# Optimization experiments

Measured on AMD Instinct MI355X. Metric: run time of the kernel, lower is better.

## Reference

```python
import jax, jax.numpy as jnp
import numpy as np

N, E, G, D, L, EA = 100000, 1600000, 128, 128, 3, 7
BN_EPS = 1e-5


def _bn(x, g, b, m, v):
    # eval-mode BatchNorm1d with running stats
    return (x - m) * (g / jnp.sqrt(v + BN_EPS)) + b


def setup_inputs() -> dict:
    key = jax.random.key(0)
    ks = iter(jax.random.split(key, 64))
    nrm = lambda shape, s: jax.random.normal(next(ks), shape, jnp.float32) * s
    unif = lambda shape: jax.random.uniform(next(ks), shape, jnp.float32) * 0.5 + 0.5
    inp = {
        # forward tensor args
        'x': jnp.zeros((N,), jnp.int32),  # indices into Embedding(1, D) -> all zero
        'edge_index': jax.random.randint(next(ks), (2, E), 0, N, jnp.int32),
        'edge_attr': nrm((E, EA), 1.0),
        'batch': jnp.sort(jax.random.randint(next(ks), (N,), 0, G, jnp.int32)),
        # embeddings
        'node_emb': nrm((1, D), 1.0),
        'vn_emb': nrm((1, D), 0.1),
        # per-layer GINConv params (stacked on leading layer dim)
        'edge_W': nrm((L, EA, D), EA ** -0.5), 'edge_b': jnp.zeros((L, D), jnp.float32),
        'eps': jnp.zeros((L,), jnp.float32),
        'mlp_W1': nrm((L, D, 2 * D), D ** -0.5), 'mlp_b1': jnp.zeros((L, 2 * D), jnp.float32),
        'mbn_g': jnp.ones((L, 2 * D), jnp.float32), 'mbn_b': jnp.zeros((L, 2 * D), jnp.float32),
        'mbn_m': nrm((L, 2 * D), 0.1), 'mbn_v': unif((L, 2 * D)),
        'mlp_W2': nrm((L, 2 * D, D), (2 * D) ** -0.5), 'mlp_b2': jnp.zeros((L, D), jnp.float32),
        # outer per-layer BatchNorm
        'bn_g': jnp.ones((L, D), jnp.float32), 'bn_b': jnp.zeros((L, D), jnp.float32),
        'bn_m': nrm((L, D), 0.1), 'bn_v': unif((L, D)),
        # virtual-node MLPs (L-1 of them)
        'vn_W1': nrm((L - 1, D, 2 * D), D ** -0.5), 'vn_b1': jnp.zeros((L - 1, 2 * D), jnp.float32),
        'vbn1_g': jnp.ones((L - 1, 2 * D), jnp.float32), 'vbn1_b': jnp.zeros((L - 1, 2 * D), jnp.float32),
        'vbn1_m': nrm((L - 1, 2 * D), 0.1), 'vbn1_v': unif((L - 1, 2 * D)),
        'vn_W2': nrm((L - 1, 2 * D, D), (2 * D) ** -0.5), 'vn_b2': jnp.zeros((L - 1, D), jnp.float32),
        'vbn2_g': jnp.ones((L - 1, D), jnp.float32), 'vbn2_b': jnp.zeros((L - 1, D), jnp.float32),
        'vbn2_m': nrm((L - 1, D), 0.1), 'vbn2_v': unif((L - 1, D)),
    }
    return inp


def reference(x, edge_index, edge_attr, batch, node_emb, vn_emb,
              edge_W, edge_b, eps, mlp_W1, mlp_b1, mbn_g, mbn_b, mbn_m, mbn_v,
              mlp_W2, mlp_b2, bn_g, bn_b, bn_m, bn_v,
              vn_W1, vn_b1, vbn1_g, vbn1_b, vbn1_m, vbn1_v,
              vn_W2, vn_b2, vbn2_g, vbn2_b, vbn2_m, vbn2_v):
    src, dst = edge_index[0], edge_index[1]
    h = node_emb[x]                                # [N, D] node encoder gather
    vn = jnp.broadcast_to(vn_emb[0], (G, D))       # virtual node per graph
    for l in range(L):
        h_in = h + vn[batch]                       # broadcast virtual node to nodes
        # GINConv
        e = edge_attr @ edge_W[l] + edge_b[l]      # [E, D]
        msg = jax.nn.relu(h_in[src] + e)           # gather + edge fuse
        agg = jax.ops.segment_sum(msg, dst, num_segments=N)
        z = (1.0 + eps[l]) * h_in + agg
        z = jax.nn.relu(_bn(z @ mlp_W1[l] + mlp_b1[l], mbn_g[l], mbn_b[l], mbn_m[l], mbn_v[l]))
        h2 = z @ mlp_W2[l] + mlp_b2[l]
        # outer BatchNorm (+ relu except last layer; dropout is identity in eval)
        h2 = _bn(h2, bn_g[l], bn_b[l], bn_m[l], bn_v[l])
        h = h2 if l == L - 1 else jax.nn.relu(h2)
        if l < L - 1:
            vt = jax.ops.segment_sum(h_in, batch, num_segments=G) + vn  # global_add_pool
            t = jax.nn.relu(_bn(vt @ vn_W1[l] + vn_b1[l], vbn1_g[l], vbn1_b[l], vbn1_m[l], vbn1_v[l]))
            vn = jax.nn.relu(_bn(t @ vn_W2[l] + vn_b2[l], vbn2_g[l], vbn2_b[l], vbn2_m[l], vbn2_v[l]))
    return h  # JK == 'last'
```

## Files before the change

### kernel.cpp

```cpp
#include <hip/hip_runtime.h>
#include <hip/hip_bf16.h>

#define NN 100000
#define NP 100032
#define EE 1600000
#define GG 128
#define DD 128
#define LL 3
#define EAA 7
#define BN_EPS 1e-5f

typedef __attribute__((ext_vector_type(8))) short bf16x8;
typedef __attribute__((ext_vector_type(4))) float f32x4;
typedef __attribute__((ext_vector_type(4))) unsigned short u16x4;

__device__ __forceinline__ unsigned short f2bf(float x) {
    unsigned int u = __float_as_uint(x);
    u = (u + 0x7FFF + ((u >> 16) & 1)) >> 16;
    return (unsigned short)u;
}
__device__ __forceinline__ float bf2f(unsigned short h) {
    return __uint_as_float(((unsigned int)h) << 16);
}
__device__ __forceinline__ float bflo(unsigned int u) {
    return __uint_as_float(u << 16);
}
__device__ __forceinline__ float bfhi(unsigned int u) {
    return __uint_as_float(u & 0xFFFF0000u);
}

__global__ __launch_bounds__(256) void init_kernel(
    const int* __restrict__ x, const float* __restrict__ node_emb,
    const float* __restrict__ vn_emb, float* __restrict__ h,
    float* __restrict__ vn)
{
    long i = (long)blockIdx.x * 256 + threadIdx.x;
    if (i < (long)NN * DD) {
        int node = (int)(i >> 7), d = (int)(i & 127);
        h[i] = node_emb[(long)x[node] * DD + d];
    }
    if (i < GG * DD) vn[i] = vn_emb[i & 127];
}

#define R1 8
__global__ __launch_bounds__(256) void hin_kernel(
    float* __restrict__ hbuf,
    unsigned short* __restrict__ h16,
    const float* __restrict__ vn,
    const int* __restrict__ batch,
    const float* __restrict__ eps,
    float* __restrict__ agg,
    float* __restrict__ vt,
    int layer, int accum_vt, int write_agg)
{
    const int d  = threadIdx.x & 127;
    const int rg = threadIdx.x >> 7;
    const float epl = 1.0f + eps[layer];
    const long row0 = (long)blockIdx.x * (R1 * 2);

    float vacc = 0.0f;
    int   vb   = -1;
    #pragma unroll
    for (int r = 0; r < R1; ++r) {
        long row = row0 + rg + 2 * r;
        if (row >= NN) break;
        int b = batch[row];
        long idx = row * DD + d;
        float hv = hbuf[idx] + vn[(long)b * DD + d];
        hbuf[idx] = hv;
        h16[idx]  = f2bf(hv);
        if (write_agg) agg[idx] = epl * hv;
        if (accum_vt) {
            if (b != vb) {
                if (vb >= 0) atomicAdd(&vt[(long)vb * DD + d], vacc);
                vb = b; vacc = 0.0f;
            }
            vacc += hv;
        }
    }
    if (accum_vt && vb >= 0) atomicAdd(&vt[(long)vb * DD + d], vacc);
}

__global__ __launch_bounds__(256) void vt_kernel(
    const float* __restrict__ hbuf, const int* __restrict__ batch,
    float* __restrict__ vt)
{
    const int d  = threadIdx.x & 127;
    const int rg = threadIdx.x >> 7;
    const long row0 = (long)blockIdx.x * 16;
    float vacc = 0.0f;
    int   vb   = -1;
    #pragma unroll
    for (int r = 0; r < 8; ++r) {
        long row = row0 + rg + 2 * r;
        if (row >= NN) break;
        int b = batch[row];
        float hv = hbuf[row * DD + d];
        if (b != vb) {
            if (vb >= 0) atomicAdd(&vt[(long)vb * DD + d], vacc);
            vb = b; vacc = 0.0f;
        }
        vacc += hv;
    }
    if (vb >= 0) atomicAdd(&vt[(long)vb * DD + d], vacc);
}

__global__ __launch_bounds__(256) void cnt_kernel(
    const int* __restrict__ batch, int* __restrict__ cnt)
{
    const int tid = blockIdx.x * 256 + threadIdx.x;
    const int CH  = (NN + 16383) / 16384;
    long s = (long)tid * CH;
    long e = s + CH; if (e > NN) e = NN;
    int vb = -1, c = 0;
    for (long i = s; i < e; ++i) {
        int b = batch[i];
        if (b != vb) { if (vb >= 0) atomicAdd(&cnt[vb], c); vb = b; c = 0; }
        ++c;
    }
    if (vb >= 0) atomicAdd(&cnt[vb], c);
}

__global__ __launch_bounds__(256) void count_kernel(
    const int* __restrict__ ei, int* __restrict__ deg)
{
    long e = (long)blockIdx.x * 256 + threadIdx.x;
    if (e < EE) atomicAdd(&deg[ei[EE + e]], 1);
}

__global__ __launch_bounds__(1024) void scan_a(
    const int* __restrict__ deg, int* __restrict__ rp, int* __restrict__ partials)
{
    __shared__ int s[1024];
    int t = threadIdx.x;
    long i = (long)blockIdx.x * 1024 + t;
    int v = (i < NN) ? deg[i] : 0;
    s[t] = v;
    __syncthreads();
    for (int off = 1; off < 1024; off <<= 1) {
        int u = (t >= off) ? s[t - off] : 0;
        __syncthreads();
        s[t] += u;
        __syncthreads();
    }
    if (i < NN) rp[i] = s[t] - v;
    if (t == 1023) partials[blockIdx.x] = s[1023];
}

__global__ void scan_b(int* __restrict__ partials, int nb)
{
    if (threadIdx.x == 0) {
        int run = 0;
        for (int i = 0; i < nb; ++i) { int v = partials[i]; partials[i] = run; run += v; }
    }
}

__global__ __launch_bounds__(1024) void scan_c(
    int* __restrict__ rp, int* __restrict__ fill, const int* __restrict__ partials)
{
    long i = (long)blockIdx.x * 1024 + threadIdx.x;
    if (i < NN) {
        int v = rp[i] + partials[blockIdx.x];
        rp[i] = v;
        fill[i] = v;
    }
    if (i == 0) rp[NN] = EE;
}

__global__ __launch_bounds__(256) void scatter_kernel(
    const int* __restrict__ ei, const float* __restrict__ eattr,
    int* __restrict__ fill, unsigned short* __restrict__ attr16,
    int* __restrict__ src_arr, int* __restrict__ eid_perm)
{
    long e = (long)blockIdx.x * 256 + threadIdx.x;
    if (e >= EE) return;
    int dst = ei[EE + e];
    int pos = atomicAdd(&fill[dst], 1);
    if (attr16) {
        u16x4 w0, w1;
        w0.x = f2bf(eattr[e * EAA + 0]);
        w0.y = f2bf(eattr[e * EAA + 1]);
        w0.z = f2bf(eattr[e * EAA + 2]);
        w0.w = f2bf(eattr[e * EAA + 3]);
        w1.x = f2bf(eattr[e * EAA + 4]);
        w1.y = f2bf(eattr[e * EAA + 5]);
        w1.z = f2bf(eattr[e * EAA + 6]);
        w1.w = 0;
        *(u16x4*)(attr16 + (long)pos * 8)     = w0;
        *(u16x4*)(attr16 + (long)pos * 8 + 4) = w1;
        src_arr[pos] = ei[e];
    } else {
        eid_perm[pos] = (int)e;
    }
}

__global__ __launch_bounds__(256) void gin0_kernel(
    const float* __restrict__ node_emb,
    const float* __restrict__ vn_emb,
    const int* __restrict__ rp,
    const unsigned short* __restrict__ attr16,
    const float* __restrict__ eW, const float* __restrict__ eb,
    const float* __restrict__ eps,
    float* __restrict__ agg)
{
    const int lane = threadIdx.x & 63;
    const int wid  = threadIdx.x >> 6;
    const long n   = (long)blockIdx.x * 4 + wid;
    const int d0   = lane * 2;

    float2 w2[EAA];
    #pragma unroll
    for (int a = 0; a < EAA; ++a)
        w2[a] = *(const float2*)&eW[a * DD + d0];
    const float2 bias = *(const float2*)&eb[d0];
    const float  epl  = 1.0f + eps[0];

    const float cx = node_emb[d0]     + vn_emb[d0];
    const float cy = node_emb[d0 + 1] + vn_emb[d0 + 1];
    float accx = epl * cx, accy = epl * cy;

    int p  = rp[n];
    const int p1 = rp[n + 1];

    #define EDGE0(AU)                                                         \
    {                                                                         \
        float a0 = bflo(AU.x), a1 = bfhi(AU.x);                               \
        float a2 = bflo(AU.y), a3 = bfhi(AU.y);                               \
        float a4 = bflo(AU.z), a5 = bfhi(AU.z);                               \
        float a6 = bflo(AU.w);                                                \
        float ex = bias.x, ey = bias.y;                                       \
        ex = fmaf(a0, w2[0].x, ex); ey = fmaf(a0, w2[0].y, ey);               \
        ex = fmaf(a1, w2[1].x, ex); ey = fmaf(a1, w2[1].y, ey);               \
        ex = fmaf(a2, w2[2].x, ex); ey = fmaf(a2, w2[2].y, ey);               \
        ex = fmaf(a3, w2[3].x, ex); ey = fmaf(a3, w2[3].y, ey);               \
        ex = fmaf(a4, w2[4].x, ex); ey = fmaf(a4, w2[4].y, ey);               \
        ex = fmaf(a5, w2[5].x, ex); ey = fmaf(a5, w2[5].y, ey);               \
        ex = fmaf(a6, w2[6].x, ex); ey = fmaf(a6, w2[6].y, ey);               \
        float mx = cx + ex, my = cy + ey;                                     \
        accx += fmaxf(mx, 0.0f); accy += fmaxf(my, 0.0f);                     \
    }

    for (; p + 4 <= p1; p += 4) {
        const uint4* a4p = (const uint4*)(attr16 + (long)p * 8);
        uint4 A0 = a4p[0];
        uint4 A1 = a4p[1];
        uint4 A2 = a4p[2];
        uint4 A3 = a4p[3];
        EDGE0(A0)
        EDGE0(A1)
        EDGE0(A2)
        EDGE0(A3)
    }
    for (; p < p1; ++p) {
        uint4 A = *(const uint4*)(attr16 + (long)p * 8);
        EDGE0(A)
    }
    #undef EDGE0

    *(float2*)&agg[n * DD + d0] = make_float2(accx, accy);
}

__global__ __launch_bounds__(256) void gin_agg_kernel(
    const float* __restrict__ h_in,
    const unsigned short* __restrict__ h16,
    const int* __restrict__ rp,
    const unsigned short* __restrict__ attr16,
    const int* __restrict__ src_arr,
    const float* __restrict__ eW, const float* __restrict__ eb,
    const float* __restrict__ eps,
    float* __restrict__ agg, int layer)
{
    const int lane = threadIdx.x & 63;
    const int wid  = threadIdx.x >> 6;
    const long n   = (long)blockIdx.x * 4 + wid;
    const int d0   = lane * 2;

    const float* eWl = eW + (long)layer * EAA * DD;
    float2 w2[EAA];
    #pragma unroll
    for (int a = 0; a < EAA; ++a)
        w2[a] = *(const float2*)&eWl[a * DD + d0];
    const float2 bias = *(const float2*)&eb[layer * DD + d0];
    const float  epl  = 1.0f + eps[layer];

    float2 hn = *(const float2*)&h_in[n * DD + d0];
    float accx = epl * hn.x, accy = epl * hn.y;

    int p  = rp[n];
    const int p1 = rp[n + 1];

    #define EDGE(AU, GU)                                                      \
    {                                                                         \
        float a0 = bflo(AU.x), a1 = bfhi(AU.x);                               \
        float a2 = bflo(AU.y), a3 = bfhi(AU.y);                               \
        float a4 = bflo(AU.z), a5 = bfhi(AU.z);                               \
        float a6 = bflo(AU.w);                                                \
        float ex = bias.x, ey = bias.y;                                       \
        ex = fmaf(a0, w2[0].x, ex); ey = fmaf(a0, w2[0].y, ey);               \
        ex = fmaf(a1, w2[1].x, ex); ey = fmaf(a1, w2[1].y, ey);               \
        ex = fmaf(a2, w2[2].x, ex); ey = fmaf(a2, w2[2].y, ey);               \
        ex = fmaf(a3, w2[3].x, ex); ey = fmaf(a3, w2[3].y, ey);               \
        ex = fmaf(a4, w2[4].x, ex); ey = fmaf(a4, w2[4].y, ey);               \
        ex = fmaf(a5, w2[5].x, ex); ey = fmaf(a5, w2[5].y, ey);               \
        ex = fmaf(a6, w2[6].x, ex); ey = fmaf(a6, w2[6].y, ey);               \
        float mx = bflo(GU) + ex, my = bfhi(GU) + ey;                         \
        accx += fmaxf(mx, 0.0f); accy += fmaxf(my, 0.0f);                     \
    }

    for (; p + 4 <= p1; p += 4) {
        int s0 = src_arr[p];
        int s1 = src_arr[p + 1];
        int s2 = src_arr[p + 2];
        int s3 = src_arr[p + 3];
        const uint4* a4p = (const uint4*)(attr16 + (long)p * 8);
        uint4 A0 = a4p[0];
        uint4 A1 = a4p[1];
        uint4 A2 = a4p[2];
        uint4 A3 = a4p[3];
        unsigned int g0 = *(const unsigned int*)(h16 + (long)s0 * DD + d0);
        unsigned int g1 = *(const unsigned int*)(h16 + (long)s1 * DD + d0);
        unsigned int g2 = *(const unsigned int*)(h16 + (long)s2 * DD + d0);
        unsigned int g3 = *(const unsigned int*)(h16 + (long)s3 * DD + d0);
        EDGE(A0, g0)
        EDGE(A1, g1)
        EDGE(A2, g2)
        EDGE(A3, g3)
    }
    for (; p < p1; ++p) {
        int s = src_arr[p];
        uint4 A = *(const uint4*)(attr16 + (long)p * 8);
        unsigned int g = *(const unsigned int*)(h16 + (long)s * DD + d0);
        EDGE(A, g)
    }
    #undef EDGE

    *(float2*)&agg[n * DD + d0] = make_float2(accx, accy);
}

__global__ __launch_bounds__(256) void gin_agg_eid_kernel(
    const float* __restrict__ h_in,
    const int* __restrict__ rp,
    const int* __restrict__ eid_perm,
    const int* __restrict__ ei,
    const float* __restrict__ eattr,
    const float* __restrict__ eW, const float* __restrict__ eb,
    const float* __restrict__ eps,
    float* __restrict__ agg, int layer)
{
    const int d    = threadIdx.x & 127;
    const int half = threadIdx.x >> 7;
    const long n   = (long)blockIdx.x * 2 + half;

    float w[EAA];
    #pragma unroll
    for (int a = 0; a < EAA; ++a) w[a] = eW[layer * EAA * DD + a * DD + d];
    const float bias = eb[layer * DD + d];
    const float epl  = 1.0f + eps[layer];

    float acc = epl * h_in[n * DD + d];
    const int p0 = rp[n], p1 = rp[n + 1];
    for (int p = p0; p < p1; ++p) {
        int e = eid_perm[p];
        int src = ei[e];
        float ea = bias;
        #pragma unroll
        for (int a = 0; a < EAA; ++a)
            ea = fmaf(eattr[(long)e * EAA + a], w[a], ea);
        float m = h_in[(long)src * DD + d] + ea;
        acc += m > 0.0f ? m : 0.0f;
    }
    agg[n * DD + d] = acc;
}

#define EPB 64
__global__ __launch_bounds__(256) void edge_kernel(
    const float* __restrict__ h_in,
    const int* __restrict__ ei,
    const float* __restrict__ eattr,
    const float* __restrict__ eW,
    const float* __restrict__ eb,
    float* __restrict__ agg,
    int layer)
{
    const int d    = threadIdx.x & 127;
    const int esub = threadIdx.x >> 7;
    float w[EAA];
    #pragma unroll
    for (int a = 0; a < EAA; ++a) w[a] = eW[layer * EAA * DD + a * DD + d];
    const float bias = eb[layer * DD + d];

    const long base = (long)blockIdx.x * EPB;
    for (int k = esub; k < EPB; k += 2) {
        long e = base + k;
        if (e >= EE) break;
        int s = ei[e];
        int t = ei[EE + e];
        float acc = bias;
        #pragma unroll
        for (int a = 0; a < EAA; ++a)
            acc = fmaf(eattr[e * EAA + a], w[a], acc);
        float m = h_in[(long)s * DD + d] + acc;
        m = m > 0.0f ? m : 0.0f;
        atomicAdd(&agg[(long)t * DD + d], m);
    }
}

__global__ __launch_bounds__(256) void wprep_kernel(
    const float* __restrict__ W1, const float* __restrict__ W2,
    unsigned short* __restrict__ w1h, unsigned short* __restrict__ w1l,
    unsigned short* __restrict__ w2h, unsigned short* __restrict__ w2l)
{
    int tid = blockIdx.x * 256 + threadIdx.x;
    if (tid >= LL * 2 * 32768) return;
    int l = tid / 65536;
    int rem = tid - l * 65536;
    int mat = rem >> 15;
    int fi = rem & 32767;
    int b = fi & 7, lane = (fi >> 3) & 63;
    int kgrp = ((lane >> 4) << 3) + b;
    if (mat == 0) {
        int mt = (fi >> 9) & 15, kk = fi >> 13;
        int m = (mt << 4) + (lane & 15);
        int k = (kk << 5) + kgrp;
        float v = W1[(long)l * DD * 2 * DD + (long)k * 2 * DD + m];
        unsigned short hi = f2bf(v);
        w1h[(long)l * 32768 + fi] = hi;
        w1l[(long)l * 32768 + fi] = f2bf(v - bf2f(hi));
    } else {
        int mt = (fi >> 9) & 7, kk = fi >> 12;
        int m = (mt << 4) + (lane & 15);
        int k = (kk << 5) + kgrp;
        float v = W2[(long)l * 2 * DD * DD + (long)k * DD + m];
        unsigned short hi = f2bf(v);
        w2h[(long)l * 32768 + fi] = hi;
        w2l[(long)l * 32768 + fi] = f2bf(v - bf2f(hi));
    }
}

__global__ __launch_bounds__(256) void bnprep_kernel(
    const float* __restrict__ b1, const float* __restrict__ g1,
    const float* __restrict__ be1, const float* __restrict__ m1,
    const float* __restrict__ v1,
    const float* __restrict__ b2, const float* __restrict__ g2,
    const float* __restrict__ be2, const float* __restrict__ m2,
    const float* __restrict__ v2,
    float* __restrict__ sc1, float* __restrict__ sh1,
    float* __restrict__ sc2, float* __restrict__ sh2)
{
    int tid = blockIdx.x * 256 + threadIdx.x;
    if (tid < LL * 2 * DD) {
        float sc = g1[tid] / sqrtf(v1[tid] + BN_EPS);
        sc1[tid] = sc;
        sh1[tid] = (b1[tid] - m1[tid]) * sc + be1[tid];
    }
    int t2 = tid - LL * 2 * DD;
    if (t2 >= 0 && t2 < LL * DD) {
        float sc = g2[t2] / sqrtf(v2[t2] + BN_EPS);
        sc2[t2] = sc;
        sh2[t2] = (b2[t2] - m2[t2]) * sc + be2[t2];
    }
}

__global__ __launch_bounds__(256, 2) void mlp_mfma_kernel(
    const float* __restrict__ z_in,
    const unsigned short* __restrict__ w1h, const unsigned short* __restrict__ w1l,
    const unsigned short* __restrict__ w2h, const unsigned short* __restrict__ w2l,
    const float* __restrict__ sc1, const float* __restrict__ sh1,
    const float* __restrict__ sc2, const float* __restrict__ sh2,
    float* __restrict__ h_out, int layer, int do_relu,
    const int* __restrict__ batch, const float* __restrict__ vnbuf,
    unsigned short* __restrict__ h16, int fuse)
{
    __shared__ char lds[65536];
    const int tid  = threadIdx.x;
    const int lane = tid & 63;
    const int wv   = tid >> 6;
    const long row0 = (long)blockIdx.x * 64;
    const int kb = (lane >> 4) << 3;

    {
        const float4* zi = (const float4*)(z_in + row0 * DD);
        #pragma unroll
        for (int i = 0; i < 8; ++i) {
            int idx = tid + i * 256;
            float4 v = zi[idx];
            int r = idx >> 5;
            int c = (idx & 31) << 2;
            u16x4 hv, lv;
            hv.x = f2bf(v.x); lv.x = f2bf(v.x - bf2f(hv.x));
            hv.y = f2bf(v.y); lv.y = f2bf(v.y - bf2f(hv.y));
            hv.z = f2bf(v.z); lv.z = f2bf(v.z - bf2f(hv.z));
            hv.w = f2bf(v.w); lv.w = f2bf(v.w - bf2f(hv.w));
            int off = ((r << 8) + (c << 1)) ^ ((r & 7) << 4);
            *(u16x4*)(lds + off)         = hv;
            *(u16x4*)(lds + 16384 + off) = lv;
        }
    }
    __syncthreads();

    bf16x8 B1h[4][4], B1l[4][4];
    #pragma unroll
    for (int nt = 0; nt < 4; ++nt) {
        int r = (nt << 4) + (lane & 15);
        #pragma unroll
        for (int kk = 0; kk < 4; ++kk) {
            int off = ((r << 8) + (((kk << 5) + kb) << 1)) ^ ((r & 7) << 4);
            B1h[nt][kk] = *(const bf16x8*)(lds + off);
            B1l[nt][kk] = *(const bf16x8*)(lds + 16384 + off);
        }
    }
    __syncthreads();

    const unsigned short* w1hl = w1h + (long)layer * 32768;
    const unsigned short* w1ll = w1l + (long)layer * 32768;
    #pragma unroll
    for (int mtl = 0; mtl < 4; ++mtl) {
        const int mt = (wv << 2) + mtl;
        bf16x8 Ah[4], Al[4];
        #pragma unroll
        for (int kk = 0; kk < 4; ++kk) {
            const long boff = ((long)((kk << 4) + mt) * 64 + lane) << 3;
            Ah[kk] = *(const bf16x8*)(w1hl + boff);
            Al[kk] = *(const bf16x8*)(w1ll + boff);
        }
        f32x4 acc[4];
        #pragma unroll
        for (int nt = 0; nt < 4; ++nt) acc[nt] = (f32x4){0.f, 0.f, 0.f, 0.f};
        #pragma unroll
        for (int kk = 0; kk < 4; ++kk) {
            #pragma unroll
            for (int nt = 0; nt < 4; ++nt) {
                acc[nt] = __builtin_amdgcn_mfma_f32_16x16x32_bf16(Ah[kk], B1h[nt][kk], acc[nt], 0, 0, 0);
                acc[nt] = __builtin_amdgcn_mfma_f32_16x16x32_bf16(Ah[kk], B1l[nt][kk], acc[nt], 0, 0, 0);
                acc[nt] = __builtin_amdgcn_mfma_f32_16x16x32_bf16(Al[kk], B1h[nt][kk], acc[nt], 0, 0, 0);
            }
        }
        const int m0 = (mt << 4) + ((lane >> 4) << 2);
        const float4 s4 = *(const float4*)&sc1[layer * 2 * DD + m0];
        const float4 t4 = *(const float4*)&sh1[layer * 2 * DD + m0];
        #pragma unroll
        for (int nt = 0; nt < 4; ++nt) {
            int row = (nt << 4) + (lane & 15);
            float u0 = fmaxf(fmaf(acc[nt][0], s4.x, t4.x), 0.0f);
            float u1 = fmaxf(fmaf(acc[nt][1], s4.y, t4.y), 0.0f);
            float u2 = fmaxf(fmaf(acc[nt][2], s4.z, t4.z), 0.0f);
            float u3 = fmaxf(fmaf(acc[nt][3], s4.w, t4.w), 0.0f);
            u16x4 hv, lv;
            hv.x = f2bf(u0); lv.x = f2bf(u0 - bf2f(hv.x));
            hv.y = f2bf(u1); lv.y = f2bf(u1 - bf2f(hv.y));
            hv.z = f2bf(u2); lv.z = f2bf(u2 - bf2f(hv.z));
            hv.w = f2bf(u3); lv.w = f2bf(u3 - bf2f(hv.w));
            int off = ((row << 9) + (m0 << 1)) ^ ((row & 7) << 4);
            *(u16x4*)(lds + off)         = hv;
            *(u16x4*)(lds + 32768 + off) = lv;
        }
    }
    __syncthreads();

    const unsigned short* w2hl = w2h + (long)layer * 32768;
    const unsigned short* w2ll = w2l + (long)layer * 32768;
    f32x4 acc2[2][4];
    #pragma unroll
    for (int mtl = 0; mtl < 2; ++mtl)
        #pragma unroll
        for (int nt = 0; nt < 4; ++nt) acc2[mtl][nt] = (f32x4){0.f, 0.f, 0.f, 0.f};

    #pragma unroll
    for (int kk = 0; kk < 8; ++kk) {
        bf16x8 Bh[4], Bl[4];
        #pragma unroll
        for (int nt = 0; nt < 4; ++nt) {
            int r = (nt << 4) + (lane & 15);
            int off = ((r << 9) + (((kk << 5) + kb) << 1)) ^ ((r & 7) << 4);
            Bh[nt] = *(const bf16x8*)(lds + off);
            Bl[nt] = *(const bf16x8*)(lds + 32768 + off);
        }
        #pragma unroll
        for (int mtl = 0; mtl < 2; ++mtl) {
            const int mt = (wv << 1) + mtl;
            const long boff = ((long)((kk << 3) + mt) * 64 + lane) << 3;
            bf16x8 Ah = *(const bf16x8*)(w2hl + boff);
            bf16x8 Al = *(const bf16x8*)(w2ll + boff);
            #pragma unroll
            for (int nt = 0; nt < 4; ++nt) {
                acc2[mtl][nt] = __builtin_amdgcn_mfma_f32_16x16x32_bf16(Ah, Bh[nt], acc2[mtl][nt], 0, 0, 0);
                acc2[mtl][nt] = __builtin_amdgcn_mfma_f32_16x16x32_bf16(Ah, Bl[nt], acc2[mtl][nt], 0, 0, 0);
                acc2[mtl][nt] = __builtin_amdgcn_mfma_f32_16x16x32_bf16(Al, Bh[nt], acc2[mtl][nt], 0, 0, 0);
            }
        }
    }
    #pragma unroll
    for (int mtl = 0; mtl < 2; ++mtl) {
        const int m0 = ((((wv << 1) + mtl)) << 4) + ((lane >> 4) << 2);
        const float4 s4 = *(const float4*)&sc2[layer * DD + m0];
        const float4 t4 = *(const float4*)&sh2[layer * DD + m0];
        #pragma unroll
        for (int nt = 0; nt < 4; ++nt) {
            long row = row0 + (nt << 4) + (lane & 15);
            if (row < NN) {
                float o0 = fmaf(acc2[mtl][nt][0], s4.x, t4.x);
                float o1 = fmaf(acc2[mtl][nt][1], s4.y, t4.y);
                float o2 = fmaf(acc2[mtl][nt][2], s4.z, t4.z);
                float o3 = fmaf(acc2[mtl][nt][3], s4.w, t4.w);
                if (do_relu) {
                    o0 = fmaxf(o0, 0.0f); o1 = fmaxf(o1, 0.0f);
                    o2 = fmaxf(o2, 0.0f); o3 = fmaxf(o3, 0.0f);
                }
                if (fuse) {
                    int b = batch[row];
                    float4 vnv = *(const float4*)&vnbuf[(long)b * DD + m0];
                    o0 += vnv.x; o1 += vnv.y; o2 += vnv.z; o3 += vnv.w;
                    u16x4 hv;
                    hv.x = f2bf(o0); hv.y = f2bf(o1);
                    hv.z = f2bf(o2); hv.w = f2bf(o3);
                    *(u16x4*)&h16[row * DD + m0] = hv;
                }
                *(float4*)&h_out[row * DD + m0] = make_float4(o0, o1, o2, o3);
            }
        }
    }
}

__global__ __launch_bounds__(256) void vn_kernel(
    const float* __restrict__ vt, float* __restrict__ vn,
    const float* __restrict__ W1, const float* __restrict__ b1,
    const float* __restrict__ g1, const float* __restrict__ be1,
    const float* __restrict__ m1, const float* __restrict__ v1,
    const float* __restrict__ W2, const float* __restrict__ b2,
    const float* __restrict__ g2, const float* __restrict__ be2,
    const float* __restrict__ m2, const float* __restrict__ v2,
    int layer)
{
    __shared__ float row[DD];
    __shared__ float u[2 * DD];
    const int g = blockIdx.x;
    const int t = threadIdx.x;

    if (t < DD) row[t] = vt[(long)g * DD + t] + vn[(long)g * DD + t];
    __syncthreads();

    {
        const float* W = W1 + (long)layer * DD * 2 * DD;
        float acc = 0.0f;
        for (int k = 0; k < DD; ++k) acc = fmaf(row[k], W[k * 2 * DD + t], acc);
        const long o = (long)layer * 2 * DD + t;
        float sc = g1[o] / sqrtf(v1[o] + BN_EPS);
        float sh = be1[o] - m1[o] * sc;
        float val = (acc + b1[o]) * sc + sh;
        u[t] = val > 0.0f ? val : 0.0f;
    }
    __syncthreads();

    if (t < DD) {
        const float* W = W2 + (long)layer * 2 * DD * DD;
        float acc = 0.0f;
        for (int k = 0; k < 2 * DD; ++k) acc = fmaf(u[k], W[k * DD + t], acc);
        const long o = (long)layer * DD + t;
        float sc = g2[o] / sqrtf(v2[o] + BN_EPS);
        float sh = be2[o] - m2[o] * sc;
        float val = (acc + b2[o]) * sc + sh;
        vn[(long)g * DD + t] = val > 0.0f ? val : 0.0f;
    }
}

__global__ __launch_bounds__(256) void vn0_kernel(
    const int* __restrict__ cnt,
    const float* __restrict__ node_emb, const float* __restrict__ vn_emb,
    float* __restrict__ vn,
    const float* __restrict__ W1, const float* __restrict__ b1,
    const float* __restrict__ g1, const float* __restrict__ be1,
    const float* __restrict__ m1, const float* __restrict__ v1,
    const float* __restrict__ W2, const float* __restrict__ b2,
    const float* __restrict__ g2, const float* __restrict__ be2,
    const float* __restrict__ m2, const float* __restrict__ v2)
{
    __shared__ float row[DD];
    __shared__ float u[2 * DD];
    const int g = blockIdx.x;
    const int t = threadIdx.x;

    if (t < DD) {
        float c = node_emb[t] + vn_emb[t];
        row[t] = (float)cnt[g] * c + vn_emb[t];
    }
    __syncthreads();

    {
        float acc = 0.0f;
        for (int k = 0; k < DD; ++k) acc = fmaf(row[k], W1[k * 2 * DD + t], acc);
        float sc = g1[t] / sqrtf(v1[t] + BN_EPS);
        float sh = be1[t] - m1[t] * sc;
        float val = (acc + b1[t]) * sc + sh;
        u[t] = val > 0.0f ? val : 0.0f;
    }
    __syncthreads();

    if (t < DD) {
        float acc = 0.0f;
        for (int k = 0; k < 2 * DD; ++k) acc = fmaf(u[k], W2[k * DD + t], acc);
        float sc = g2[t] / sqrtf(v2[t] + BN_EPS);
        float sh = be2[t] - m2[t] * sc;
        float val = (acc + b2[t]) * sc + sh;
        vn[(long)g * DD + t] = val > 0.0f ? val : 0.0f;
    }
}

extern "C" void kernel_launch(void* const* d_in, const int* in_sizes, int n_in,
                              void* d_out, int out_size, void* d_ws, size_t ws_size,
                              hipStream_t stream)
{
    const int*   x       = (const int*)  d_in[0];
    const int*   ei      = (const int*)  d_in[1];
    const float* eattr   = (const float*)d_in[2];
    const int*   batch   = (const int*)  d_in[3];
    const float* node_emb= (const float*)d_in[4];
    const float* vn_emb  = (const float*)d_in[5];
    const float* edge_W  = (const float*)d_in[6];
    const float* edge_b  = (const float*)d_in[7];
    const float* eps     = (const float*)d_in[8];
    const float* mlp_W1  = (const float*)d_in[9];
    const float* mlp_b1  = (const float*)d_in[10];
    const float* mbn_g   = (const float*)d_in[11];
    const float* mbn_b   = (const float*)d_in[12];
    const float* mbn_m   = (const float*)d_in[13];
    const float* mbn_v   = (const float*)d_in[14];
    const float* mlp_W2  = (const float*)d_in[15];
    const float* mlp_b2  = (const float*)d_in[16];
    const float* bn_g    = (const float*)d_in[17];
    const float* bn_b    = (const float*)d_in[18];
    const float* bn_m    = (const float*)d_in[19];
    const float* bn_v    = (const float*)d_in[20];
    const float* vn_W1   = (const float*)d_in[21];
    const float* vn_b1   = (const float*)d_in[22];
    const float* vbn1_g  = (const float*)d_in[23];
    const float* vbn1_b  = (const float*)d_in[24];
    const float* vbn1_m  = (const float*)d_in[25];
    const float* vbn1_v  = (const float*)d_in[26];
    const float* vn_W2   = (const float*)d_in[27];
    const float* vn_b2   = (const float*)d_in[28];
    const float* vbn2_g  = (const float*)d_in[29];
    const float* vbn2_b  = (const float*)d_in[30];
    const float* vbn2_m  = (const float*)d_in[31];
    const float* vbn2_v  = (const float*)d_in[32];

    float* h = (float*)d_out;
    char*  ws = (char*)d_ws;

    size_t off = 0;
    auto alloc = [&](size_t bytes) -> void* {
        void* p = ws + off;
        off += (bytes + 255) & ~(size_t)255;
        return p;
    };
    const size_t GDB = (size_t)GG * DD * sizeof(float);

    float* agg      = (float*)alloc((size_t)NP * DD * sizeof(float));
    unsigned short* h16 = (unsigned short*)alloc((size_t)NN * DD * sizeof(unsigned short));
    float* vn       = (float*)alloc(GDB);
    float* vt       = (float*)alloc(GDB);
    int*   rp       = (int*)  alloc((NN + 1) * sizeof(int));
    int*   fill     = (int*)  alloc(NN * sizeof(int));
    int*   partials = (int*)  alloc(128 * sizeof(int));
    int*   cnt      = (int*)  alloc(GG * sizeof(int));
    int*   src_arr  = (int*)  alloc((size_t)EE * sizeof(int));
    unsigned short* w1h = (unsigned short*)alloc(LL * 32768 * sizeof(unsigned short));
    unsigned short* w1l = (unsigned short*)alloc(LL * 32768 * sizeof(unsigned short));
    unsigned short* w2h = (unsigned short*)alloc(LL * 32768 * sizeof(unsigned short));
    unsigned short* w2l = (unsigned short*)alloc(LL * 32768 * sizeof(unsigned short));
    float* bn1sc = (float*)alloc(LL * 2 * DD * sizeof(float));
    float* bn1sh = (float*)alloc(LL * 2 * DD * sizeof(float));
    float* bn2sc = (float*)alloc(LL * DD * sizeof(float));
    float* bn2sh = (float*)alloc(LL * DD * sizeof(float));
    const size_t base_end = off;

    unsigned short* attr16 = nullptr;
    int* eid_perm = nullptr;
    if (ws_size >= base_end + (size_t)EE * 8 * sizeof(unsigned short))
        attr16 = (unsigned short*)alloc((size_t)EE * 8 * sizeof(unsigned short));
    else if (ws_size >= base_end + (size_t)EE * sizeof(int))
        eid_perm = (int*)alloc((size_t)EE * sizeof(int));

    wprep_kernel<<<(LL * 2 * 32768 + 255) / 256, 256, 0, stream>>>(
        mlp_W1, mlp_W2, w1h, w1l, w2h, w2l);
    bnprep_kernel<<<(LL * 2 * DD + LL * DD + 255) / 256, 256, 0, stream>>>(
        mlp_b1, mbn_g, mbn_b, mbn_m, mbn_v,
        mlp_b2, bn_g, bn_b, bn_m, bn_v,
        bn1sc, bn1sh, bn2sc, bn2sh);

    const bool csr = (attr16 != nullptr) || (eid_perm != nullptr);
    if (csr) {
        const int egrid = (EE + 255) / 256;
        const int ngrid = (NN + 1023) / 1024;
        hipMemsetAsync(fill, 0, NN * sizeof(int), stream);
        count_kernel<<<egrid, 256, 0, stream>>>(ei, fill);
        scan_a<<<ngrid, 1024, 0, stream>>>(fill, rp, partials);
        scan_b<<<1, 64, 0, stream>>>(partials, ngrid);
        scan_c<<<ngrid, 1024, 0, stream>>>(rp, fill, partials);
        scatter_kernel<<<egrid, 256, 0, stream>>>(ei, eattr, fill, attr16, src_arr, eid_perm);
    }

    if (attr16) {
        hipMemsetAsync(cnt, 0, GG * sizeof(int), stream);
        cnt_kernel<<<64, 256, 0, stream>>>(batch, cnt);

        vn0_kernel<<<GG, 256, 0, stream>>>(
            cnt, node_emb, vn_emb, vn,
            vn_W1, vn_b1, vbn1_g, vbn1_b, vbn1_m, vbn1_v,
            vn_W2, vn_b2, vbn2_g, vbn2_b, vbn2_m, vbn2_v);
        gin0_kernel<<<NN / 4, 256, 0, stream>>>(
            node_emb, vn_emb, rp, attr16, edge_W, edge_b, eps, agg);
        mlp_mfma_kernel<<<NP / 64, 256, 0, stream>>>(
            agg, w1h, w1l, w2h, w2l, bn1sc, bn1sh, bn2sc, bn2sh,
            h, 0, 1, batch, vn, h16, 1);

        hipMemsetAsync(vt, 0, GDB, stream);
        vt_kernel<<<NN / 16, 256, 0, stream>>>(h, batch, vt);
        vn_kernel<<<GG, 256, 0, stream>>>(
            vt, vn, vn_W1, vn_b1, vbn1_g, vbn1_b, vbn1_m, vbn1_v,
            vn_W2, vn_b2, vbn2_g, vbn2_b, vbn2_m, vbn2_v, 1);
        gin_agg_kernel<<<NN / 4, 256, 0, stream>>>(
            h, h16, rp, attr16, src_arr, edge_W, edge_b, eps, agg, 1);
        mlp_mfma_kernel<<<NP / 64, 256, 0, stream>>>(
            agg, w1h, w1l, w2h, w2l, bn1sc, bn1sh, bn2sc, bn2sh,
            h, 1, 1, batch, vn, h16, 1);

        gin_agg_kernel<<<NN / 4, 256, 0, stream>>>(
            h, h16, rp, attr16, src_arr, edge_W, edge_b, eps, agg, 2);
        mlp_mfma_kernel<<<NP / 64, 256, 0, stream>>>(
            agg, w1h, w1l, w2h, w2l, bn1sc, bn1sh, bn2sc, bn2sh,
            h, 2, 0, batch, vn, h16, 0);
    } else {
        {
            long total = (long)NN * DD;
            init_kernel<<<(int)((total + 255) / 256), 256, 0, stream>>>(
                x, node_emb, vn_emb, h, vn);
        }
        for (int l = 0; l < LL; ++l) {
            int accum = (l < LL - 1) ? 1 : 0;
            if (accum)
                hipMemsetAsync(vt, 0, GDB, stream);

            hin_kernel<<<NN / (R1 * 2), 256, 0, stream>>>(
                h, h16, vn, batch, eps, agg, vt, l, accum, csr ? 0 : 1);

            if (eid_perm) {
                gin_agg_eid_kernel<<<NN / 2, 256, 0, stream>>>(
                    h, rp, eid_perm, ei, eattr, edge_W, edge_b, eps, agg, l);
            } else {
                edge_kernel<<<(EE + EPB - 1) / EPB, 256, 0, stream>>>(
                    h, ei, eattr, edge_W, edge_b, agg, l);
            }

            mlp_mfma_kernel<<<NP / 64, 256, 0, stream>>>(
                agg, w1h, w1l, w2h, w2l, bn1sc, bn1sh, bn2sc, bn2sh,
                h, l, accum, batch, vn, h16, 0);

            if (accum)
                vn_kernel<<<GG, 256, 0, stream>>>(
                    vt, vn, vn_W1, vn_b1, vbn1_g, vbn1_b, vbn1_m, vbn1_v,
                    vn_W2, vn_b2, vbn2_g, vbn2_b, vbn2_m, vbn2_v, l);
        }
    }
}
```

Baseline: 766.9 us.

## Use fp16 packed dot2 for edge encoding and emit split-bf16 aggregates

```diff
diff --git a/kernel.cpp b/kernel.cpp
--- a/kernel.cpp
+++ b/kernel.cpp
@@ -13,6 +13,7 @@
 typedef __attribute__((ext_vector_type(8))) short bf16x8;
 typedef __attribute__((ext_vector_type(4))) float f32x4;
 typedef __attribute__((ext_vector_type(4))) unsigned short u16x4;
+typedef _Float16 f16x2 __attribute__((ext_vector_type(2)));
 
 __device__ __forceinline__ unsigned short f2bf(float x) {
     unsigned int u = __float_as_uint(x);
@@ -28,6 +29,19 @@
 __device__ __forceinline__ float bfhi(unsigned int u) {
     return __uint_as_float(u & 0xFFFF0000u);
 }
+__device__ __forceinline__ unsigned int pkf16(float a, float b) {
+    f16x2 v = {(_Float16)a, (_Float16)b};
+    return __builtin_bit_cast(unsigned int, v);
+}
+
+#if __has_builtin(__builtin_amdgcn_fdot2)
+#define DOT2(q, w, c) __builtin_amdgcn_fdot2((q), (w), (c), false)
+#else
+__device__ __forceinline__ float dot2_sw(f16x2 a, f16x2 b, float c) {
+    return fmaf((float)a.x, (float)b.x, fmaf((float)a.y, (float)b.y, c));
+}
+#define DOT2(q, w, c) dot2_sw((q), (w), (c))
+#endif
 
 __global__ __launch_bounds__(256) void init_kernel(
     const int* __restrict__ x, const float* __restrict__ node_emb,
@@ -169,7 +183,7 @@
 
 __global__ __launch_bounds__(256) void scatter_kernel(
     const int* __restrict__ ei, const float* __restrict__ eattr,
-    int* __restrict__ fill, unsigned short* __restrict__ attr16,
+    int* __restrict__ fill, unsigned int* __restrict__ attr16,
     int* __restrict__ src_arr, int* __restrict__ eid_perm)
 {
     long e = (long)blockIdx.x * 256 + threadIdx.x;
@@ -177,41 +191,61 @@
     int dst = ei[EE + e];
     int pos = atomicAdd(&fill[dst], 1);
     if (attr16) {
-        u16x4 w0, w1;
-        w0.x = f2bf(eattr[e * EAA + 0]);
-        w0.y = f2bf(eattr[e * EAA + 1]);
-        w0.z = f2bf(eattr[e * EAA + 2]);
-        w0.w = f2bf(eattr[e * EAA + 3]);
-        w1.x = f2bf(eattr[e * EAA + 4]);
-        w1.y = f2bf(eattr[e * EAA + 5]);
-        w1.z = f2bf(eattr[e * EAA + 6]);
-        w1.w = 0;
-        *(u16x4*)(attr16 + (long)pos * 8)     = w0;
-        *(u16x4*)(attr16 + (long)pos * 8 + 4) = w1;
+        uint4 w;
+        w.x = pkf16(eattr[e * EAA + 0], eattr[e * EAA + 1]);
+        w.y = pkf16(eattr[e * EAA + 2], eattr[e * EAA + 3]);
+        w.z = pkf16(eattr[e * EAA + 4], eattr[e * EAA + 5]);
+        w.w = pkf16(eattr[e * EAA + 6], 0.0f);
+        *(uint4*)(attr16 + (long)pos * 4) = w;
         src_arr[pos] = ei[e];
     } else {
         eid_perm[pos] = (int)e;
     }
 }
+
+#define WPAIR_PREAMBLE(eWl)                                                   \
+    f16x2 wx[4], wy[4];                                                       \
+    {                                                                         \
+        _Pragma("unroll")                                                     \
+        for (int j = 0; j < 3; ++j) {                                         \
+            float2 p0 = *(const float2*)&(eWl)[(2 * j) * DD + d0];            \
+            float2 p1 = *(const float2*)&(eWl)[(2 * j + 1) * DD + d0];        \
+            wx[j] = (f16x2){(_Float16)p0.x, (_Float16)p1.x};                  \
+            wy[j] = (f16x2){(_Float16)p0.y, (_Float16)p1.y};                  \
+        }                                                                     \
+        float2 p6 = *(const float2*)&(eWl)[6 * DD + d0];                      \
+        wx[3] = (f16x2){(_Float16)p6.x, (_Float16)0.0f};                      \
+        wy[3] = (f16x2){(_Float16)p6.y, (_Float16)0.0f};                      \
+    }
+
+#define EDOT(AU, EX, EY)                                                      \
+    float EX = bias.x, EY = bias.y;                                           \
+    {                                                                         \
+        f16x2 q0 = __builtin_bit_cast(f16x2, AU.x);                           \
+        f16x2 q1 = __builtin_bit_cast(f16x2, AU.y);                           \
+        f16x2 q2 = __builtin_bit_cast(f16x2, AU.z);                           \
+        f16x2 q3 = __builtin_bit_cast(f16x2, AU.w);                           \
+        EX = DOT2(q0, wx[0], EX); EY = DOT2(q0, wy[0], EY);                   \
+        EX = DOT2(q1, wx[1], EX); EY = DOT2(q1, wy[1], EY);                   \
+        EX = DOT2(q2, wx[2], EX); EY = DOT2(q2, wy[2], EY);                   \
+        EX = DOT2(q3, wx[3], EX); EY = DOT2(q3, wy[3], EY);                   \
+    }
 
 __global__ __launch_bounds__(256) void gin0_kernel(
     const float* __restrict__ node_emb,
     const float* __restrict__ vn_emb,
     const int* __restrict__ rp,
-    const unsigned short* __restrict__ attr16,
+    const unsigned int* __restrict__ attr16,
     const float* __restrict__ eW, const float* __restrict__ eb,
     const float* __restrict__ eps,
-    float* __restrict__ agg)
+    unsigned short* __restrict__ aggh, unsigned short* __restrict__ aggl)
 {
     const int lane = threadIdx.x & 63;
     const int wid  = threadIdx.x >> 6;
     const long n   = (long)blockIdx.x * 4 + wid;
     const int d0   = lane * 2;
 
-    float2 w2[EAA];
-    #pragma unroll
-    for (int a = 0; a < EAA; ++a)
-        w2[a] = *(const float2*)&eW[a * DD + d0];
+    WPAIR_PREAMBLE(eW)
     const float2 bias = *(const float2*)&eb[d0];
     const float  epl  = 1.0f + eps[0];
 
@@ -224,24 +258,13 @@
 
     #define EDGE0(AU)                                                         \
     {                                                                         \
-        float a0 = bflo(AU.x), a1 = bfhi(AU.x);                               \
-        float a2 = bflo(AU.y), a3 = bfhi(AU.y);                               \
-        float a4 = bflo(AU.z), a5 = bfhi(AU.z);                               \
-        float a6 = bflo(AU.w);                                                \
-        float ex = bias.x, ey = bias.y;                                       \
-        ex = fmaf(a0, w2[0].x, ex); ey = fmaf(a0, w2[0].y, ey);               \
-        ex = fmaf(a1, w2[1].x, ex); ey = fmaf(a1, w2[1].y, ey);               \
-        ex = fmaf(a2, w2[2].x, ex); ey = fmaf(a2, w2[2].y, ey);               \
-        ex = fmaf(a3, w2[3].x, ex); ey = fmaf(a3, w2[3].y, ey);               \
-        ex = fmaf(a4, w2[4].x, ex); ey = fmaf(a4, w2[4].y, ey);               \
-        ex = fmaf(a5, w2[5].x, ex); ey = fmaf(a5, w2[5].y, ey);               \
-        ex = fmaf(a6, w2[6].x, ex); ey = fmaf(a6, w2[6].y, ey);               \
+        EDOT(AU, ex, ey)                                                      \
         float mx = cx + ex, my = cy + ey;                                     \
         accx += fmaxf(mx, 0.0f); accy += fmaxf(my, 0.0f);                     \
     }
 
     for (; p + 4 <= p1; p += 4) {
-        const uint4* a4p = (const uint4*)(attr16 + (long)p * 8);
+        const uint4* a4p = (const uint4*)(attr16 + (long)p * 4);
         uint4 A0 = a4p[0];
         uint4 A1 = a4p[1];
         uint4 A2 = a4p[2];
@@ -252,23 +275,27 @@
         EDGE0(A3)
     }
     for (; p < p1; ++p) {
-        uint4 A = *(const uint4*)(attr16 + (long)p * 8);
+        uint4 A = *(const uint4*)(attr16 + (long)p * 4);
         EDGE0(A)
     }
     #undef EDGE0
 
-    *(float2*)&agg[n * DD + d0] = make_float2(accx, accy);
+    unsigned short hx = f2bf(accx), hy = f2bf(accy);
+    *(unsigned int*)&aggh[n * DD + d0] = (unsigned int)hx | ((unsigned int)hy << 16);
+    *(unsigned int*)&aggl[n * DD + d0] =
+        (unsigned int)f2bf(accx - bf2f(hx)) | ((unsigned int)f2bf(accy - bf2f(hy)) << 16);
 }
 
 __global__ __launch_bounds__(256) void gin_agg_kernel(
     const float* __restrict__ h_in,
     const unsigned short* __restrict__ h16,
     const int* __restrict__ rp,
-    const unsigned short* __restrict__ attr16,
+    const unsigned int* __restrict__ attr16,
     const int* __restrict__ src_arr,
     const float* __restrict__ eW, const float* __restrict__ eb,
     const float* __restrict__ eps,
-    float* __restrict__ agg, int layer)
+    unsigned short* __restrict__ aggh, unsigned short* __restrict__ aggl,
+    int layer)
 {
     const int lane = threadIdx.x & 63;
     const int wid  = threadIdx.x >> 6;
@@ -276,10 +303,7 @@
     const int d0   = lane * 2;
 
     const float* eWl = eW + (long)layer * EAA * DD;
-    float2 w2[EAA];
-    #pragma unroll
-    for (int a = 0; a < EAA; ++a)
-        w2[a] = *(const float2*)&eWl[a * DD + d0];
+    WPAIR_PREAMBLE(eWl)
     const float2 bias = *(const float2*)&eb[layer * DD + d0];
     const float  epl  = 1.0f + eps[layer];
 
@@ -291,18 +315,7 @@
 
     #define EDGE(AU, GU)                                                      \
     {                                                                         \
-        float a0 = bflo(AU.x), a1 = bfhi(AU.x);                               \
-        float a2 = bflo(AU.y), a3 = bfhi(AU.y);                               \
-        float a4 = bflo(AU.z), a5 = bfhi(AU.z);                               \
-        float a6 = bflo(AU.w);                                                \
-        float ex = bias.x, ey = bias.y;                                       \
-        ex = fmaf(a0, w2[0].x, ex); ey = fmaf(a0, w2[0].y, ey);               \
-        ex = fmaf(a1, w2[1].x, ex); ey = fmaf(a1, w2[1].y, ey);               \
-        ex = fmaf(a2, w2[2].x, ex); ey = fmaf(a2, w2[2].y, ey);               \
-        ex = fmaf(a3, w2[3].x, ex); ey = fmaf(a3, w2[3].y, ey);               \
-        ex = fmaf(a4, w2[4].x, ex); ey = fmaf(a4, w2[4].y, ey);               \
-        ex = fmaf(a5, w2[5].x, ex); ey = fmaf(a5, w2[5].y, ey);               \
-        ex = fmaf(a6, w2[6].x, ex); ey = fmaf(a6, w2[6].y, ey);               \
+        EDOT(AU, ex, ey)                                                      \
         float mx = bflo(GU) + ex, my = bfhi(GU) + ey;                         \
         accx += fmaxf(mx, 0.0f); accy += fmaxf(my, 0.0f);                     \
     }
@@ -312,7 +325,7 @@
         int s1 = src_arr[p + 1];
         int s2 = src_arr[p + 2];
         int s3 = src_arr[p + 3];
-        const uint4* a4p = (const uint4*)(attr16 + (long)p * 8);
+        const uint4* a4p = (const uint4*)(attr16 + (long)p * 4);
         uint4 A0 = a4p[0];
         uint4 A1 = a4p[1];
         uint4 A2 = a4p[2];
@@ -328,13 +341,16 @@
     }
     for (; p < p1; ++p) {
         int s = src_arr[p];
-        uint4 A = *(const uint4*)(attr16 + (long)p * 8);
+        uint4 A = *(const uint4*)(attr16 + (long)p * 4);
         unsigned int g = *(const unsigned int*)(h16 + (long)s * DD + d0);
         EDGE(A, g)
     }
     #undef EDGE
 
-    *(float2*)&agg[n * DD + d0] = make_float2(accx, accy);
+    unsigned short hx = f2bf(accx), hy = f2bf(accy);
+    *(unsigned int*)&aggh[n * DD + d0] = (unsigned int)hx | ((unsigned int)hy << 16);
+    *(unsigned int*)&aggl[n * DD + d0] =
+        (unsigned int)f2bf(accx - bf2f(hx)) | ((unsigned int)f2bf(accy - bf2f(hy)) << 16);
 }
 
 __global__ __launch_bounds__(256) void gin_agg_eid_kernel(
@@ -463,6 +479,8 @@
 
 __global__ __launch_bounds__(256, 2) void mlp_mfma_kernel(
     const float* __restrict__ z_in,
+    const unsigned short* __restrict__ z16h, const unsigned short* __restrict__ z16l,
+    int zfmt,
     const unsigned short* __restrict__ w1h, const unsigned short* __restrict__ w1l,
     const unsigned short* __restrict__ w2h, const unsigned short* __restrict__ w2l,
     const float* __restrict__ sc1, const float* __restrict__ sh1,
@@ -478,7 +496,21 @@
     const long row0 = (long)blockIdx.x * 64;
     const int kb = (lane >> 4) << 3;
 
-    {
+    if (zfmt) {
+        const uint4* zh = (const uint4*)(z16h + row0 * DD);
+        const uint4* zl = (const uint4*)(z16l + row0 * DD);
+        #pragma unroll
+        for (int i = 0; i < 4; ++i) {
+            int idx = tid + i * 256;
+            uint4 hv = zh[idx];
+            uint4 lv = zl[idx];
+            int r = idx >> 4;
+            int c = (idx & 15) << 3;
+            int off = ((r << 8) + (c << 1)) ^ ((r & 7) << 4);
+            *(uint4*)(lds + off)         = hv;
+            *(uint4*)(lds + 16384 + off) = lv;
+        }
+    } else {
         const float4* zi = (const float4*)(z_in + row0 * DD);
         #pragma unroll
         for (int i = 0; i < 8; ++i) {
@@ -755,6 +787,8 @@
     const size_t GDB = (size_t)GG * DD * sizeof(float);
 
     float* agg      = (float*)alloc((size_t)NP * DD * sizeof(float));
+    unsigned short* aggh = (unsigned short*)agg;
+    unsigned short* aggl = aggh + (size_t)NP * DD;
     unsigned short* h16 = (unsigned short*)alloc((size_t)NN * DD * sizeof(unsigned short));
     float* vn       = (float*)alloc(GDB);
     float* vt       = (float*)alloc(GDB);
@@ -773,10 +807,10 @@
     float* bn2sh = (float*)alloc(LL * DD * sizeof(float));
     const size_t base_end = off;
 
-    unsigned short* attr16 = nullptr;
+    unsigned int* attr16 = nullptr;
     int* eid_perm = nullptr;
-    if (ws_size >= base_end + (size_t)EE * 8 * sizeof(unsigned short))
-        attr16 = (unsigned short*)alloc((size_t)EE * 8 * sizeof(unsigned short));
+    if (ws_size >= base_end + (size_t)EE * 4 * sizeof(unsigned int))
+        attr16 = (unsigned int*)alloc((size_t)EE * 4 * sizeof(unsigned int));
     else if (ws_size >= base_end + (size_t)EE * sizeof(int))
         eid_perm = (int*)alloc((size_t)EE * sizeof(int));
 
@@ -808,9 +842,9 @@
             vn_W1, vn_b1, vbn1_g, vbn1_b, vbn1_m, vbn1_v,
             vn_W2, vn_b2, vbn2_g, vbn2_b, vbn2_m, vbn2_v);
         gin0_kernel<<<NN / 4, 256, 0, stream>>>(
-            node_emb, vn_emb, rp, attr16, edge_W, edge_b, eps, agg);
+            node_emb, vn_emb, rp, attr16, edge_W, edge_b, eps, aggh, aggl);
         mlp_mfma_kernel<<<NP / 64, 256, 0, stream>>>(
-            agg, w1h, w1l, w2h, w2l, bn1sc, bn1sh, bn2sc, bn2sh,
+            agg, aggh, aggl, 1, w1h, w1l, w2h, w2l, bn1sc, bn1sh, bn2sc, bn2sh,
             h, 0, 1, batch, vn, h16, 1);
 
         hipMemsetAsync(vt, 0, GDB, stream);
@@ -819,15 +853,15 @@
             vt, vn, vn_W1, vn_b1, vbn1_g, vbn1_b, vbn1_m, vbn1_v,
             vn_W2, vn_b2, vbn2_g, vbn2_b, vbn2_m, vbn2_v, 1);
         gin_agg_kernel<<<NN / 4, 256, 0, stream>>>(
-            h, h16, rp, attr16, src_arr, edge_W, edge_b, eps, agg, 1);
+            h, h16, rp, attr16, src_arr, edge_W, edge_b, eps, aggh, aggl, 1);
         mlp_mfma_kernel<<<NP / 64, 256, 0, stream>>>(
-            agg, w1h, w1l, w2h, w2l, bn1sc, bn1sh, bn2sc, bn2sh,
+            agg, aggh, aggl, 1, w1h, w1l, w2h, w2l, bn1sc, bn1sh, bn2sc, bn2sh,
             h, 1, 1, batch, vn, h16, 1);
 
         gin_agg_kernel<<<NN / 4, 256, 0, stream>>>(
-            h, h16, rp, attr16, src_arr, edge_W, edge_b, eps, agg, 2);
+            h, h16, rp, attr16, src_arr, edge_W, edge_b, eps, aggh, aggl, 2);
         mlp_mfma_kernel<<<NP / 64, 256, 0, stream>>>(
-            agg, w1h, w1l, w2h, w2l, bn1sc, bn1sh, bn2sc, bn2sh,
+            agg, aggh, aggl, 1, w1h, w1l, w2h, w2l, bn1sc, bn1sh, bn2sc, bn2sh,
             h, 2, 0, batch, vn, h16, 0);
     } else {
         {
@@ -841,7 +875,7 @@
                 hipMemsetAsync(vt, 0, GDB, stream);
 
             hin_kernel<<<NN / (R1 * 2), 256, 0, stream>>>(
-                h, h16, vn, batch, eps, agg, vt, l, accum, csr ? 0 : 1);
+                h, h16, vn, batch, eps, agg, vt, l, accum, 1);
 
             if (eid_perm) {
                 gin_agg_eid_kernel<<<NN / 2, 256, 0, stream>>>(
@@ -852,7 +886,8 @@
             }
 
             mlp_mfma_kernel<<<NP / 64, 256, 0, stream>>>(
-                agg, w1h, w1l, w2h, w2l, bn1sc, bn1sh, bn2sc, bn2sh,
+                agg, nullptr, nullptr, 0, w1h, w1l, w2h, w2l,
+                bn1sc, bn1sh, bn2sc, bn2sh,
                 h, l, accum, batch, vn, h16, 0);
 
             if (accum)
```

Result: faster. 743.1 us (-3.1%).
